# Kernel tuning notes

Hardware: AMD Instinct MI355X
Metric: run time of the kernel (lower is better)

Reference implementation:

```python
import jax, jax.numpy as jnp
import numpy as np
import math

B, S, HID, NH = 2, 1024, 4096, 32
HD = HID // NH  # 128


def setup_inputs() -> dict:
    key = jax.random.key(0)
    ks = jax.random.split(key, 6)
    scale = 0.02
    x = jax.random.normal(ks[0], (B, S, HID), dtype=jnp.float32)
    Wq = jax.random.normal(ks[1], (HID, HID), dtype=jnp.float32) * scale
    Wk = jax.random.normal(ks[2], (HID, HID), dtype=jnp.float32) * scale
    Wv = jax.random.normal(ks[3], (HID, HID), dtype=jnp.float32) * scale
    Wo = jax.random.normal(ks[4], (HID, HID), dtype=jnp.float32) * scale
    bq = jnp.zeros((HID,), jnp.float32)
    bk = jnp.zeros((HID,), jnp.float32)
    bv = jnp.zeros((HID,), jnp.float32)
    bo = jnp.zeros((HID,), jnp.float32)
    position_ids = jnp.tile(jnp.arange(S, dtype=jnp.int32)[None, :], (B, 1))
    # additive causal mask: 0 on/below diagonal, large negative above
    causal = jnp.tril(jnp.ones((S, S), dtype=bool))
    attention_mask = jnp.where(causal, 0.0, -1e9).astype(jnp.float32)[None, None]
    return {"x": x, "Wq": Wq, "bq": bq, "Wk": Wk, "bk": bk, "Wv": Wv,
            "bv": bv, "Wo": Wo, "bo": bo, "position_ids": position_ids,
            "attention_mask": attention_mask}


def _rotate_interleaved(t):
    # stack([-t[..., 1::2], t[..., ::2]], -1).reshape_as(t)
    return jnp.stack([-t[..., 1::2], t[..., ::2]], axis=-1).reshape(t.shape)


def reference(x, Wq, bq, Wk, bk, Wv, bv, Wo, bo, position_ids, attention_mask):
    b, s, _ = x.shape
    q = x @ Wq.T + bq
    k = x @ Wk.T + bk
    v = x @ Wv.T + bv
    # [B, NH, S, HD]
    q = q.reshape(b, s, NH, HD).transpose(0, 2, 1, 3)
    k = k.reshape(b, s, NH, HD).transpose(0, 2, 1, 3)
    v = v.reshape(b, s, NH, HD).transpose(0, 2, 1, 3)
    # RoPE (interleaved pairs), cos/sin recomputed each call as in source
    inv_freq = 1.0 / (10000.0 ** (jnp.arange(0, HD, 2, dtype=jnp.float32) / HD))
    ang = position_ids.astype(jnp.float32)[..., None] * inv_freq  # [B,S,HD/2]
    cos = jnp.repeat(jnp.cos(ang), 2, axis=-1)[:, None]  # [B,1,S,HD]
    sin = jnp.repeat(jnp.sin(ang), 2, axis=-1)[:, None]
    q = q * cos + _rotate_interleaved(q) * sin
    k = k * cos + _rotate_interleaved(k) * sin
    # naive full attention
    scores = jnp.einsum('bhqd,bhkd->bhqk', q, k) / math.sqrt(HD)
    scores = scores + attention_mask
    probs = jax.nn.softmax(scores, axis=-1)
    out = jnp.einsum('bhqk,bhkd->bhqd', probs, v)
    out = out.transpose(0, 2, 1, 3).reshape(b, s, HID)
    return out @ Wo.T + bo
```

## Files before the change

kernel.cpp:

```cpp
#include <hip/hip_runtime.h>
#include <hip/hip_bf16.h>
#include <cmath>

constexpr int cB  = 2;
constexpr int cS  = 1024;
constexpr int cNH = 32;
constexpr int cHD = 128;
constexpr int cHID = 4096;
constexpr int cM  = cB * cS;

typedef unsigned short u16;
typedef __bf16 bf16x8 __attribute__((ext_vector_type(8)));
typedef float  f32x4  __attribute__((ext_vector_type(4)));

__device__ __forceinline__ u16 f2b(float f) { return __builtin_bit_cast(u16, (__bf16)f); }

__global__ void cvt_bf16(const float* __restrict__ in, u16* __restrict__ out, int n8) {
  int i = blockIdx.x * blockDim.x + threadIdx.x;
  if (i >= n8) return;
  const float4* in4 = (const float4*)in;
  float4 a = in4[2 * i], b = in4[2 * i + 1];
  union { u16 u[8]; uint4 v; } r;
  r.u[0] = f2b(a.x); r.u[1] = f2b(a.y); r.u[2] = f2b(a.z); r.u[3] = f2b(a.w);
  r.u[4] = f2b(b.x); r.u[5] = f2b(b.y); r.u[6] = f2b(b.z); r.u[7] = f2b(b.w);
  ((uint4*)out)[i] = r.v;
}

__global__ void rope_table_k(const int* __restrict__ pos,
                             float* __restrict__ cosT, float* __restrict__ sinT) {
  int idx = blockIdx.x * blockDim.x + threadIdx.x;
  int i = idx & 63, bs = idx >> 6;
  float p = (float)pos[bs];
  float freq = exp2f(-(float)i * (13.287712379549449f / 64.0f));
  float a = p * freq;
  float s, c;
  sincosf(a, &s, &c);
  cosT[idx] = c; sinT[idx] = s;
}

__global__ void rope_apply(u16* __restrict__ Q, u16* __restrict__ Kb,
                           const float* __restrict__ cosT, const float* __restrict__ sinT) {
  int idx = blockIdx.x * blockDim.x + threadIdx.x;
  const int nPer = cB * cS * cNH * (cHD / 8);
  u16* P = (idx < nPer) ? Q : Kb;
  int t = (idx < nPer) ? idx : idx - nPer;
  int d8 = t & 15;
  int h  = (t >> 4) & 31;
  int bs = t >> 9;
  size_t base = ((size_t)bs * cNH + h) * cHD + d8 * 8;
  uint4 v = *reinterpret_cast<uint4*>(P + base);
  u16* u = reinterpret_cast<u16*>(&v);
  int pb = bs * 64 + d8 * 4;
  float4 cs = *reinterpret_cast<const float4*>(cosT + pb);
  float4 sn = *reinterpret_cast<const float4*>(sinT + pb);
  float co[4] = {cs.x, cs.y, cs.z, cs.w};
  float si[4] = {sn.x, sn.y, sn.z, sn.w};
#pragma unroll
  for (int p = 0; p < 4; ++p) {
    float e = (float)__builtin_bit_cast(__bf16, u[2 * p]);
    float o = (float)__builtin_bit_cast(__bf16, u[2 * p + 1]);
    float e2 = e * co[p] - o * si[p];
    float o2 = o * co[p] + e * si[p];
    u[2 * p]     = f2b(e2);
    u[2 * p + 1] = f2b(o2);
  }
  *reinterpret_cast<uint4*>(P + base) = v;
}

__global__ void transpose_v(const u16* __restrict__ V, u16* __restrict__ Vt) {
  __shared__ u16 tile[32][33];
  int bh = blockIdx.z;
  int b = bh >> 5, h = bh & 31;
  int s0 = blockIdx.x * 32, d0 = blockIdx.y * 32;
  int tx = threadIdx.x & 31, ty0 = threadIdx.x >> 5;
#pragma unroll
  for (int i = 0; i < 4; ++i) {
    int r = ty0 + i * 8;
    tile[r][tx] = V[((size_t)(b * cS + s0 + r) * cNH + h) * cHD + d0 + tx];
  }
  __syncthreads();
#pragma unroll
  for (int i = 0; i < 4; ++i) {
    int r = ty0 + i * 8;
    Vt[((size_t)bh * cHD + d0 + r) * cS + s0 + tx] = tile[tx][r];
  }
}

template <int MODE>
__global__ __launch_bounds__(256)
void gemm_bt(const u16* __restrict__ A,
             const u16* __restrict__ W0, const u16* __restrict__ W1,
             const u16* __restrict__ W2,
             const float* __restrict__ b0, const float* __restrict__ b1,
             const float* __restrict__ b2,
             void* o0, void* o1, void* o2, int kLen) {
  __shared__ __align__(16) u16 sA[2][128 * 64];
  __shared__ __align__(16) u16 sB[2][128 * 64];
  const int tid = threadIdx.x;
  const int w = tid >> 6, lane = tid & 63;
  const int c = lane & 15, g = lane >> 4;
  const int m0 = blockIdx.x * 128;
  const int gn0 = blockIdx.y * 128;
  const int sel = gn0 >> 12;
  const int n0 = gn0 & 4095;
  const u16* Bw = (sel == 0) ? W0 : (sel == 1 ? W1 : W2);
  const int k0 = blockIdx.z * kLen;
  const int wm = w >> 1, wn = w & 1;

  f32x4 acc[4][4] = {};
  const int nkt = kLen >> 6;

#define STAGE(kt, buf)                                                         \
  {                                                                            \
    _Pragma("unroll") for (int j = 0; j < 4; ++j) {                            \
      int chunk = (j * 4 + w) * 64 + lane;                                     \
      int row = chunk >> 3, lc = chunk & 7;                                    \
      __builtin_amdgcn_global_load_lds(                                        \
          (const void*)(A + (size_t)(m0 + row) * cHID + k0 + (kt) * 64 + lc * 8), \
          (void*)(sA[buf] + (size_t)(j * 4 + w) * 512), 16, 0, 0);             \
      __builtin_amdgcn_global_load_lds(                                        \
          (const void*)(Bw + (size_t)(n0 + row) * cHID + k0 + (kt) * 64 + lc * 8), \
          (void*)(sB[buf] + (size_t)(j * 4 + w) * 512), 16, 0, 0);             \
    }                                                                          \
  }

  STAGE(0, 0);
  __syncthreads();

  for (int kt = 0; kt < nkt; ++kt) {
    const int buf = kt & 1;
    if (kt + 1 < nkt) STAGE(kt + 1, buf ^ 1);

    bf16x8 af[2][4], bfr[2][4];
#pragma unroll
    for (int kf = 0; kf < 2; ++kf) {
#pragma unroll
      for (int f = 0; f < 4; ++f) {
        int ra = wm * 64 + f * 16 + c;
        af[kf][f] = *reinterpret_cast<const bf16x8*>(sA[buf] + ra * 64 + (kf * 4 + g) * 8);
        int rb = wn * 64 + f * 16 + c;
        bfr[kf][f] = *reinterpret_cast<const bf16x8*>(sB[buf] + rb * 64 + (kf * 4 + g) * 8);
      }
    }
#pragma unroll
    for (int kf = 0; kf < 2; ++kf)
#pragma unroll
      for (int mf = 0; mf < 4; ++mf)
#pragma unroll
        for (int nf = 0; nf < 4; ++nf)
          acc[mf][nf] = __builtin_amdgcn_mfma_f32_16x16x32_bf16(af[kf][mf], bfr[kf][nf], acc[mf][nf], 0, 0, 0);

    __syncthreads();
  }
#undef STAGE

  const float* bp = (sel == 0) ? b0 : (sel == 1 ? b1 : b2);
  void* op = (sel == 0) ? o0 : (sel == 1 ? o1 : o2);
  float* fp = (float*)op;
  if (MODE == 2) fp += (size_t)blockIdx.z * cM * cHID;

#pragma unroll
  for (int nf = 0; nf < 4; ++nf) {
    int col = n0 + wn * 64 + nf * 16 + c;
    float bv = (MODE == 2) ? 0.f : bp[col];
#pragma unroll
    for (int mf = 0; mf < 4; ++mf) {
      int row = m0 + wm * 64 + mf * 16 + g * 4;
#pragma unroll
      for (int r = 0; r < 4; ++r) {
        float v = acc[mf][nf][r] + bv;
        if (MODE == 0)
          ((u16*)op)[(size_t)(row + r) * cHID + col] = f2b(v);
        else
          fp[(size_t)(row + r) * cHID + col] = v;
      }
    }
  }
}

__global__ void combine_bias(const float* __restrict__ P,
                             const float* __restrict__ bias,
                             float* __restrict__ out) {
  int i = blockIdx.x * blockDim.x + threadIdx.x;
  float4 a = ((const float4*)P)[i];
  float4 b = ((const float4*)P)[i + (cM * cHID / 4)];
  int col4 = (i & (cHID / 4 - 1)) * 4;
  float4 bb = *reinterpret_cast<const float4*>(bias + col4);
  float4 r;
  r.x = a.x + b.x + bb.x; r.y = a.y + b.y + bb.y;
  r.z = a.z + b.z + bb.z; r.w = a.w + b.w + bb.w;
  ((float4*)out)[i] = r;
}

__global__ __launch_bounds__(256, 2)
void attn_kernel(const u16* __restrict__ Q, const u16* __restrict__ Kb,
                 const u16* __restrict__ Vt, u16* __restrict__ O) {
  __shared__ __align__(16) char sK[2][16384];
  __shared__ __align__(16) char sV[2][16384];
  __shared__ __align__(16) char sP[8192];
  const int tid = threadIdx.x, w = tid >> 6, lane = tid & 63;
  const int c = lane & 15, g = lane >> 4;
  const int bh = blockIdx.y;
  const int b = bh >> 5, h = bh & 31;
  const int NT = cS / 64;
  const int qtA = blockIdx.x, qtB = NT - 1 - blockIdx.x;
  const float kSc = 0.12751744f;

  bf16x8 qf[2][4];
#pragma unroll
  for (int s = 0; s < 2; ++s) {
    int q0s = (s ? qtA : qtB) * 64;
    size_t qrow = ((size_t)(b * cS + q0s + w * 16 + c) * cNH + h) * cHD;
#pragma unroll
    for (int df = 0; df < 4; ++df)
      qf[s][df] = *reinterpret_cast<const bf16x8*>(Q + qrow + df * 32 + g * 8);
  }

  f32x4 o[2][8] = {};
  float mx[2][4], ls[2][4];
#pragma unroll
  for (int s = 0; s < 2; ++s)
#pragma unroll
    for (int r = 0; r < 4; ++r) { mx[s][r] = -1e30f; ls[s][r] = 0.f; }

  uint4 kv[4], vv[4];
#define LOADT(t)                                                               \
  {                                                                            \
    _Pragma("unroll") for (int i = 0; i < 4; ++i) {                            \
      int cidx = i * 256 + tid;                                                \
      { int row = cidx >> 4, ch = cidx & 15;                                   \
        kv[i] = *reinterpret_cast<const uint4*>(                               \
            Kb + ((size_t)(b * cS + (t) * 64 + row) * cNH + h) * cHD + ch * 8); } \
      { int row = cidx >> 3, ch = cidx & 7;                                    \
        vv[i] = *reinterpret_cast<const uint4*>(                               \
            Vt + ((size_t)bh * cHD + row) * cS + (t) * 64 + ch * 8); }         \
    }                                                                          \
  }
#define WRITET(buf)                                                            \
  {                                                                            \
    _Pragma("unroll") for (int i = 0; i < 4; ++i) {                            \
      int cidx = i * 256 + tid;                                                \
      { int row = cidx >> 4, ch = cidx & 15;                                   \
        *reinterpret_cast<uint4*>(sK[buf] + row * 256 + ((ch ^ (row & 7)) * 16)) = kv[i]; } \
      { int row = cidx >> 3, ch = cidx & 7;                                    \
        *reinterpret_cast<uint4*>(sV[buf] + row * 128 + ((ch ^ (row & 7)) * 16)) = vv[i]; } \
    }                                                                          \
  }

  LOADT(0);
  WRITET(0);
  int cur = 0;

  for (int t = 0; t <= qtB; ++t) {
    __syncthreads();
    if (t < qtB) LOADT(t + 1);

#pragma unroll
    for (int s = 0; s < 2; ++s) {
      const int qt_s = s ? qtA : qtB;
      if (t > qt_s) continue;
      const int q0_s = qt_s * 64;

      f32x4 sc[4] = {};
#pragma unroll
      for (int df = 0; df < 4; ++df) {
        bf16x8 kb[4];
#pragma unroll
        for (int cf = 0; cf < 4; ++cf) {
          int kr = cf * 16 + c;
          kb[cf] = *reinterpret_cast<const bf16x8*>(sK[cur] + kr * 256 + (((df * 4 + g) ^ (kr & 7)) * 16));
        }
#pragma unroll
        for (int cf = 0; cf < 4; ++cf)
          sc[cf] = __builtin_amdgcn_mfma_f32_16x16x32_bf16(qf[s][df], kb[cf], sc[cf], 0, 0, 0);
      }

      if (t == qt_s) {
#pragma unroll
        for (int cf = 0; cf < 4; ++cf) {
          int kg = t * 64 + cf * 16 + c;
#pragma unroll
          for (int r = 0; r < 4; ++r) {
            int qg = q0_s + w * 16 + g * 4 + r;
            if (kg > qg) sc[cf][r] = -1e30f;
          }
        }
      }

      float alpha[4];
#pragma unroll
      for (int r = 0; r < 4; ++r) {
        float v = fmaxf(fmaxf(sc[0][r], sc[1][r]), fmaxf(sc[2][r], sc[3][r]));
        v = fmaxf(v, __shfl_xor(v, 1));
        v = fmaxf(v, __shfl_xor(v, 2));
        v = fmaxf(v, __shfl_xor(v, 4));
        v = fmaxf(v, __shfl_xor(v, 8));
        float mn = fmaxf(mx[s][r], v);
        alpha[r] = exp2f((mx[s][r] - mn) * kSc);
        mx[s][r] = mn;
      }
      float rs[4] = {0.f, 0.f, 0.f, 0.f};
#pragma unroll
      for (int cf = 0; cf < 4; ++cf)
#pragma unroll
        for (int r = 0; r < 4; ++r) {
          float p = exp2f((sc[cf][r] - mx[s][r]) * kSc);
          sc[cf][r] = p;
          rs[r] += p;
        }
#pragma unroll
      for (int r = 0; r < 4; ++r) {
        float v = rs[r];
        v += __shfl_xor(v, 1); v += __shfl_xor(v, 2);
        v += __shfl_xor(v, 4); v += __shfl_xor(v, 8);
        ls[s][r] = ls[s][r] * alpha[r] + v;
      }
#pragma unroll
      for (int nf = 0; nf < 8; ++nf)
#pragma unroll
        for (int r = 0; r < 4; ++r)
          o[s][nf][r] *= alpha[r];

      char* myP = sP + w * 2048;
#pragma unroll
      for (int cf = 0; cf < 4; ++cf) {
        int kcol = cf * 16 + c;
        int chunk = kcol >> 3, within = kcol & 7;
#pragma unroll
        for (int r = 0; r < 4; ++r) {
          int qr = g * 4 + r;
          *reinterpret_cast<u16*>(myP + qr * 128 + ((chunk ^ (qr & 7)) * 16) + within * 2) =
              f2b(sc[cf][r]);
        }
      }
      bf16x8 pa[2];
#pragma unroll
      for (int kf = 0; kf < 2; ++kf)
        pa[kf] = *reinterpret_cast<const bf16x8*>(myP + c * 128 + (((kf * 4 + g) ^ (c & 7)) * 16));

#pragma unroll
      for (int kf = 0; kf < 2; ++kf) {
#pragma unroll
        for (int nf = 0; nf < 8; ++nf) {
          int dr = nf * 16 + c;
          bf16x8 vb = *reinterpret_cast<const bf16x8*>(sV[cur] + dr * 128 + (((kf * 4 + g) ^ (dr & 7)) * 16));
          o[s][nf] = __builtin_amdgcn_mfma_f32_16x16x32_bf16(pa[kf], vb, o[s][nf], 0, 0, 0);
        }
      }
    }

    if (t < qtB) { WRITET(cur ^ 1); cur ^= 1; }
  }

  __syncthreads();
#pragma unroll
  for (int s = 0; s < 2; ++s) {
#pragma unroll
    for (int nf = 0; nf < 8; ++nf) {
#pragma unroll
      for (int r = 0; r < 4; ++r) {
        float v = o[s][nf][r] / ls[s][r];
        int qr = w * 16 + g * 4 + r;
        *reinterpret_cast<u16*>(sK[s] + qr * 256 + (nf * 16 + c) * 2) = f2b(v);
      }
    }
  }
  __syncthreads();
#pragma unroll
  for (int s = 0; s < 2; ++s) {
    int q0_s = (s ? qtA : qtB) * 64;
#pragma unroll
    for (int i = 0; i < 4; ++i) {
      int cidx = i * 256 + tid;
      int row = cidx >> 4, ch = cidx & 15;
      uint4 v = *reinterpret_cast<const uint4*>(sK[s] + row * 256 + ch * 16);
      *reinterpret_cast<uint4*>(O + ((size_t)(b * cS + q0_s + row) * cNH + h) * cHD + ch * 8) = v;
    }
  }
#undef LOADT
#undef WRITET
}

extern "C" void kernel_launch(void* const* d_in, const int* in_sizes, int n_in,
                              void* d_out, int out_size, void* d_ws, size_t ws_size,
                              hipStream_t stream) {
  const float* x  = (const float*)d_in[0];
  const float* Wq = (const float*)d_in[1];
  const float* bq = (const float*)d_in[2];
  const float* Wk = (const float*)d_in[3];
  const float* bk = (const float*)d_in[4];
  const float* Wv = (const float*)d_in[5];
  const float* bv = (const float*)d_in[6];
  const float* Wo = (const float*)d_in[7];
  const float* bo = (const float*)d_in[8];
  const int*  pos = (const int*)d_in[9];
  float* out = (float*)d_out;

  char* ws = (char*)d_ws;
  const size_t MB = 1u << 20;
  const int W8 = (cHID * cHID) / 8;
  const int X8 = (cM * cHID) / 8;
  const int R8 = cB * cS * cNH * (cHD / 8);

  if (ws_size >= 168 * MB) {
    u16* xb  = (u16*)(ws);
    u16* Qb  = (u16*)(ws + 16 * MB);
    u16* Kb  = (u16*)(ws + 32 * MB);
    u16* Vb  = (u16*)(ws + 48 * MB);
    float* cosT = (float*)(ws + 64 * MB);
    float* sinT = cosT + cB * cS * 64;
    u16* WbQ = (u16*)(ws + 72 * MB);
    u16* WbK = (u16*)(ws + 104 * MB);
    u16* WbV = (u16*)(ws + 136 * MB);
    u16* Vt  = WbQ;
    u16* Ab  = WbK;
    u16* WbO = WbV;
    float* P01 = (float*)(ws);

    cvt_bf16<<<X8 / 256, 256, 0, stream>>>(x, xb, X8);
    cvt_bf16<<<W8 / 256, 256, 0, stream>>>(Wq, WbQ, W8);
    cvt_bf16<<<W8 / 256, 256, 0, stream>>>(Wk, WbK, W8);
    cvt_bf16<<<W8 / 256, 256, 0, stream>>>(Wv, WbV, W8);
    rope_table_k<<<(cB * cS * 64) / 256, 256, 0, stream>>>(pos, cosT, sinT);

    gemm_bt<0><<<dim3(16, 96), 256, 0, stream>>>(
        xb, WbQ, WbK, WbV, bq, bk, bv, Qb, Kb, Vb, cHID);

    rope_apply<<<(2 * R8) / 256, 256, 0, stream>>>(Qb, Kb, cosT, sinT);
    transpose_v<<<dim3(cS / 32, cHD / 32, cB * cNH), 256, 0, stream>>>(Vb, Vt);
    attn_kernel<<<dim3(cS / 128, cB * cNH), 256, 0, stream>>>(Qb, Kb, Vt, Ab);

    cvt_bf16<<<W8 / 256, 256, 0, stream>>>(Wo, WbO, W8);
    gemm_bt<2><<<dim3(16, 32, 2), 256, 0, stream>>>(
        Ab, WbO, WbO, WbO, nullptr, nullptr, nullptr, P01, P01, P01, cHID / 2);
    combine_bias<<<(cM * cHID / 4) / 256, 256, 0, stream>>>(P01, bo, out);
  } else {
    u16* xb = (u16*)(ws);
    u16* Wb = (u16*)(ws + 16 * MB);
    u16* Qb = (u16*)(ws + 48 * MB);
    u16* Kb = (u16*)(ws + 64 * MB);
    u16* Vb = (u16*)(ws + 80 * MB);
    u16* Vt = xb;
    u16* Ab = Vb;
    float* cosT = (float*)(ws + 96 * MB);
    float* sinT = cosT + cB * cS * 64;

    cvt_bf16<<<X8 / 256, 256, 0, stream>>>(x, xb, X8);
    cvt_bf16<<<W8 / 256, 256, 0, stream>>>(Wq, Wb, W8);
    gemm_bt<0><<<dim3(16, 32), 256, 0, stream>>>(
        xb, Wb, Wb, Wb, bq, bq, bq, Qb, Qb, Qb, cHID);
    cvt_bf16<<<W8 / 256, 256, 0, stream>>>(Wk, Wb, W8);
    gemm_bt<0><<<dim3(16, 32), 256, 0, stream>>>(
        xb, Wb, Wb, Wb, bk, bk, bk, Kb, Kb, Kb, cHID);
    cvt_bf16<<<W8 / 256, 256, 0, stream>>>(Wv, Wb, W8);
    gemm_bt<0><<<dim3(16, 32), 256, 0, stream>>>(
        xb, Wb, Wb, Wb, bv, bv, bv, Vb, Vb, Vb, cHID);

    rope_table_k<<<(cB * cS * 64) / 256, 256, 0, stream>>>(pos, cosT, sinT);
    rope_apply<<<(2 * R8) / 256, 256, 0, stream>>>(Qb, Kb, cosT, sinT);
    transpose_v<<<dim3(cS / 32, cHD / 32, cB * cNH), 256, 0, stream>>>(Vb, Vt);
    attn_kernel<<<dim3(cS / 128, cB * cNH), 256, 0, stream>>>(Qb, Kb, Vt, Ab);

    cvt_bf16<<<W8 / 256, 256, 0, stream>>>(Wo, Wb, W8);
    gemm_bt<1><<<dim3(16, 32), 256, 0, stream>>>(
        Ab, Wb, Wb, Wb, bo, bo, bo, out, out, out, cHID);
  }
}
```

Measured before the change: 550.4 us.

## Rewrite GEMM as 8-wave 128x256 tile with swizzled LDS and split-phase pipeline

Replaces the 256-thread 128x128 GEMM with a 512-thread, 8-wave kernel on 128x256 tiles. LDS chunks are XOR-swizzled to avoid bank conflicts. The main loop waits with explicit vmcnt/lgkmcnt, raw barriers and setprio, and splits the MFMA work into two halves so the second B-fragment reads overlap the first MFMAs. The output projection drops split-K and the combine_bias pass and writes the fp32 result with bias directly, which cuts an extra kernel and its memory traffic but leaves fewer blocks (256) for that GEMM.

```diff
diff --git a/kernel.cpp b/kernel.cpp
--- a/kernel.cpp
+++ b/kernel.cpp
@@ -87,82 +87,117 @@
 }
 
 template <int MODE>
-__global__ __launch_bounds__(256)
-void gemm_bt(const u16* __restrict__ A,
-             const u16* __restrict__ W0, const u16* __restrict__ W1,
-             const u16* __restrict__ W2,
-             const float* __restrict__ b0, const float* __restrict__ b1,
-             const float* __restrict__ b2,
-             void* o0, void* o1, void* o2, int kLen) {
+__global__ __launch_bounds__(512, 2)
+void gemm8(const u16* __restrict__ A,
+           const u16* __restrict__ W0, const u16* __restrict__ W1,
+           const u16* __restrict__ W2,
+           const float* __restrict__ b0, const float* __restrict__ b1,
+           const float* __restrict__ b2,
+           void* o0, void* o1, void* o2) {
   __shared__ __align__(16) u16 sA[2][128 * 64];
-  __shared__ __align__(16) u16 sB[2][128 * 64];
+  __shared__ __align__(16) u16 sB[2][256 * 64];
   const int tid = threadIdx.x;
-  const int w = tid >> 6, lane = tid & 63;
+  const int wid = tid >> 6, lane = tid & 63;
   const int c = lane & 15, g = lane >> 4;
+  const int wm = wid >> 2, wn = wid & 3;
   const int m0 = blockIdx.x * 128;
-  const int gn0 = blockIdx.y * 128;
+  const int gn0 = blockIdx.y * 256;
   const int sel = gn0 >> 12;
   const int n0 = gn0 & 4095;
   const u16* Bw = (sel == 0) ? W0 : (sel == 1 ? W1 : W2);
-  const int k0 = blockIdx.z * kLen;
-  const int wm = w >> 1, wn = w & 1;
 
   f32x4 acc[4][4] = {};
-  const int nkt = kLen >> 6;
-
-#define STAGE(kt, buf)                                                         \
+  const int nkt = cHID / 64;
+
+#define STAGE8(kt, bf)                                                         \
   {                                                                            \
-    _Pragma("unroll") for (int j = 0; j < 4; ++j) {                            \
-      int chunk = (j * 4 + w) * 64 + lane;                                     \
-      int row = chunk >> 3, lc = chunk & 7;                                    \
+    _Pragma("unroll") for (int l = 0; l < 2; ++l) {                            \
+      int chunk = (l * 8 + wid) * 64 + lane;                                   \
+      int row = chunk >> 3, kc = (chunk & 7) ^ (row & 7);                      \
       __builtin_amdgcn_global_load_lds(                                        \
-          (const void*)(A + (size_t)(m0 + row) * cHID + k0 + (kt) * 64 + lc * 8), \
-          (void*)(sA[buf] + (size_t)(j * 4 + w) * 512), 16, 0, 0);             \
+          (const void*)(A + (size_t)(m0 + row) * cHID + (kt) * 64 + kc * 8),   \
+          (void*)(&sA[bf][(l * 8 + wid) * 512]), 16, 0, 0);                    \
+    }                                                                          \
+    _Pragma("unroll") for (int l = 0; l < 4; ++l) {                            \
+      int chunk = (l * 8 + wid) * 64 + lane;                                   \
+      int row = chunk >> 3, kc = (chunk & 7) ^ (row & 7);                      \
       __builtin_amdgcn_global_load_lds(                                        \
-          (const void*)(Bw + (size_t)(n0 + row) * cHID + k0 + (kt) * 64 + lc * 8), \
-          (void*)(sB[buf] + (size_t)(j * 4 + w) * 512), 16, 0, 0);             \
+          (const void*)(Bw + (size_t)(n0 + row) * cHID + (kt) * 64 + kc * 8),  \
+          (void*)(&sB[bf][(l * 8 + wid) * 512]), 16, 0, 0);                    \
     }                                                                          \
   }
 
-  STAGE(0, 0);
-  __syncthreads();
-
+  STAGE8(0, 0);
   for (int kt = 0; kt < nkt; ++kt) {
     const int buf = kt & 1;
-    if (kt + 1 < nkt) STAGE(kt + 1, buf ^ 1);
-
-    bf16x8 af[2][4], bfr[2][4];
-#pragma unroll
-    for (int kf = 0; kf < 2; ++kf) {
-#pragma unroll
-      for (int f = 0; f < 4; ++f) {
-        int ra = wm * 64 + f * 16 + c;
-        af[kf][f] = *reinterpret_cast<const bf16x8*>(sA[buf] + ra * 64 + (kf * 4 + g) * 8);
-        int rb = wn * 64 + f * 16 + c;
-        bfr[kf][f] = *reinterpret_cast<const bf16x8*>(sB[buf] + rb * 64 + (kf * 4 + g) * 8);
-      }
+    if (kt + 1 < nkt) {
+      STAGE8(kt + 1, buf ^ 1);
+      asm volatile("s_waitcnt vmcnt(6)" ::: "memory");
+    } else {
+      asm volatile("s_waitcnt vmcnt(0)" ::: "memory");
     }
-#pragma unroll
-    for (int kf = 0; kf < 2; ++kf)
+    __builtin_amdgcn_sched_barrier(0);
+    __builtin_amdgcn_s_barrier();
+
+    bf16x8 a[4][2], b[2][2];
+#pragma unroll
+    for (int mf = 0; mf < 4; ++mf)
+#pragma unroll
+      for (int kk = 0; kk < 2; ++kk) {
+        int ra = wm * 64 + mf * 16 + c;
+        a[mf][kk] = *reinterpret_cast<const bf16x8*>(
+            &sA[buf][ra * 64 + (((kk * 4 + g) ^ (ra & 7)) * 8)]);
+      }
+#pragma unroll
+    for (int nf = 0; nf < 2; ++nf)
+#pragma unroll
+      for (int kk = 0; kk < 2; ++kk) {
+        int rb = wn * 64 + nf * 16 + c;
+        b[nf][kk] = *reinterpret_cast<const bf16x8*>(
+            &sB[buf][rb * 64 + (((kk * 4 + g) ^ (rb & 7)) * 8)]);
+      }
+    __builtin_amdgcn_s_barrier();
+    asm volatile("s_waitcnt lgkmcnt(0)" ::: "memory");
+    __builtin_amdgcn_sched_barrier(0);
+    __builtin_amdgcn_s_setprio(1);
+#pragma unroll
+    for (int kk = 0; kk < 2; ++kk)
 #pragma unroll
       for (int mf = 0; mf < 4; ++mf)
 #pragma unroll
-        for (int nf = 0; nf < 4; ++nf)
-          acc[mf][nf] = __builtin_amdgcn_mfma_f32_16x16x32_bf16(af[kf][mf], bfr[kf][nf], acc[mf][nf], 0, 0, 0);
-
-    __syncthreads();
-  }
-#undef STAGE
+        for (int nf = 0; nf < 2; ++nf)
+          acc[mf][nf] = __builtin_amdgcn_mfma_f32_16x16x32_bf16(a[mf][kk], b[nf][kk], acc[mf][nf], 0, 0, 0);
+    __builtin_amdgcn_s_setprio(0);
+
+#pragma unroll
+    for (int nf = 0; nf < 2; ++nf)
+#pragma unroll
+      for (int kk = 0; kk < 2; ++kk) {
+        int rb = wn * 64 + (nf + 2) * 16 + c;
+        b[nf][kk] = *reinterpret_cast<const bf16x8*>(
+            &sB[buf][rb * 64 + (((kk * 4 + g) ^ (rb & 7)) * 8)]);
+      }
+    asm volatile("s_waitcnt lgkmcnt(0)" ::: "memory");
+    __builtin_amdgcn_sched_barrier(0);
+    __builtin_amdgcn_s_barrier();
+    __builtin_amdgcn_s_setprio(1);
+#pragma unroll
+    for (int kk = 0; kk < 2; ++kk)
+#pragma unroll
+      for (int mf = 0; mf < 4; ++mf)
+#pragma unroll
+        for (int nf = 0; nf < 2; ++nf)
+          acc[mf][nf + 2] = __builtin_amdgcn_mfma_f32_16x16x32_bf16(a[mf][kk], b[nf][kk], acc[mf][nf + 2], 0, 0, 0);
+    __builtin_amdgcn_s_setprio(0);
+  }
+#undef STAGE8
 
   const float* bp = (sel == 0) ? b0 : (sel == 1 ? b1 : b2);
   void* op = (sel == 0) ? o0 : (sel == 1 ? o1 : o2);
-  float* fp = (float*)op;
-  if (MODE == 2) fp += (size_t)blockIdx.z * cM * cHID;
-
 #pragma unroll
   for (int nf = 0; nf < 4; ++nf) {
     int col = n0 + wn * 64 + nf * 16 + c;
-    float bv = (MODE == 2) ? 0.f : bp[col];
+    float bv = bp[col];
 #pragma unroll
     for (int mf = 0; mf < 4; ++mf) {
       int row = m0 + wm * 64 + mf * 16 + g * 4;
@@ -172,24 +207,10 @@
         if (MODE == 0)
           ((u16*)op)[(size_t)(row + r) * cHID + col] = f2b(v);
         else
-          fp[(size_t)(row + r) * cHID + col] = v;
+          ((float*)op)[(size_t)(row + r) * cHID + col] = v;
       }
     }
   }
-}
-
-__global__ void combine_bias(const float* __restrict__ P,
-                             const float* __restrict__ bias,
-                             float* __restrict__ out) {
-  int i = blockIdx.x * blockDim.x + threadIdx.x;
-  float4 a = ((const float4*)P)[i];
-  float4 b = ((const float4*)P)[i + (cM * cHID / 4)];
-  int col4 = (i & (cHID / 4 - 1)) * 4;
-  float4 bb = *reinterpret_cast<const float4*>(bias + col4);
-  float4 r;
-  r.x = a.x + b.x + bb.x; r.y = a.y + b.y + bb.y;
-  r.z = a.z + b.z + bb.z; r.w = a.w + b.w + bb.w;
-  ((float4*)out)[i] = r;
 }
 
 __global__ __launch_bounds__(256, 2)
@@ -415,7 +436,6 @@
     u16* Vt  = WbQ;
     u16* Ab  = WbK;
     u16* WbO = WbV;
-    float* P01 = (float*)(ws);
 
     cvt_bf16<<<X8 / 256, 256, 0, stream>>>(x, xb, X8);
     cvt_bf16<<<W8 / 256, 256, 0, stream>>>(Wq, WbQ, W8);
@@ -423,17 +443,16 @@
     cvt_bf16<<<W8 / 256, 256, 0, stream>>>(Wv, WbV, W8);
     rope_table_k<<<(cB * cS * 64) / 256, 256, 0, stream>>>(pos, cosT, sinT);
 
-    gemm_bt<0><<<dim3(16, 96), 256, 0, stream>>>(
-        xb, WbQ, WbK, WbV, bq, bk, bv, Qb, Kb, Vb, cHID);
+    gemm8<0><<<dim3(16, 48), 512, 0, stream>>>(
+        xb, WbQ, WbK, WbV, bq, bk, bv, Qb, Kb, Vb);
 
     rope_apply<<<(2 * R8) / 256, 256, 0, stream>>>(Qb, Kb, cosT, sinT);
     transpose_v<<<dim3(cS / 32, cHD / 32, cB * cNH), 256, 0, stream>>>(Vb, Vt);
     attn_kernel<<<dim3(cS / 128, cB * cNH), 256, 0, stream>>>(Qb, Kb, Vt, Ab);
 
     cvt_bf16<<<W8 / 256, 256, 0, stream>>>(Wo, WbO, W8);
-    gemm_bt<2><<<dim3(16, 32, 2), 256, 0, stream>>>(
-        Ab, WbO, WbO, WbO, nullptr, nullptr, nullptr, P01, P01, P01, cHID / 2);
-    combine_bias<<<(cM * cHID / 4) / 256, 256, 0, stream>>>(P01, bo, out);
+    gemm8<1><<<dim3(16, 16), 512, 0, stream>>>(
+        Ab, WbO, WbO, WbO, bo, bo, bo, out, out, out);
   } else {
     u16* xb = (u16*)(ws);
     u16* Wb = (u16*)(ws + 16 * MB);
@@ -447,14 +466,14 @@
 
     cvt_bf16<<<X8 / 256, 256, 0, stream>>>(x, xb, X8);
     cvt_bf16<<<W8 / 256, 256, 0, stream>>>(Wq, Wb, W8);
-    gemm_bt<0><<<dim3(16, 32), 256, 0, stream>>>(
-        xb, Wb, Wb, Wb, bq, bq, bq, Qb, Qb, Qb, cHID);
+    gemm8<0><<<dim3(16, 16), 512, 0, stream>>>(
+        xb, Wb, Wb, Wb, bq, bq, bq, Qb, Qb, Qb);
     cvt_bf16<<<W8 / 256, 256, 0, stream>>>(Wk, Wb, W8);
-    gemm_bt<0><<<dim3(16, 32), 256, 0, stream>>>(
-        xb, Wb, Wb, Wb, bk, bk, bk, Kb, Kb, Kb, cHID);
+    gemm8<0><<<dim3(16, 16), 512, 0, stream>>>(
+        xb, Wb, Wb, Wb, bk, bk, bk, Kb, Kb, Kb);
     cvt_bf16<<<W8 / 256, 256, 0, stream>>>(Wv, Wb, W8);
-    gemm_bt<0><<<dim3(16, 32), 256, 0, stream>>>(
-        xb, Wb, Wb, Wb, bv, bv, bv, Vb, Vb, Vb, cHID);
+    gemm8<0><<<dim3(16, 16), 512, 0, stream>>>(
+        xb, Wb, Wb, Wb, bv, bv, bv, Vb, Vb, Vb);
 
     rope_table_k<<<(cB * cS * 64) / 256, 256, 0, stream>>>(pos, cosT, sinT);
     rope_apply<<<(2 * R8) / 256, 256, 0, stream>>>(Qb, Kb, cosT, sinT);
@@ -462,7 +481,7 @@
     attn_kernel<<<dim3(cS / 128, cB * cNH), 256, 0, stream>>>(Qb, Kb, Vt, Ab);
 
     cvt_bf16<<<W8 / 256, 256, 0, stream>>>(Wo, Wb, W8);
-    gemm_bt<1><<<dim3(16, 32), 256, 0, stream>>>(
-        Ab, Wb, Wb, Wb, bo, bo, bo, out, out, out, cHID);
-  }
-}
+    gemm8<1><<<dim3(16, 16), 512, 0, stream>>>(
+        Ab, Wb, Wb, Wb, bo, bo, bo, out, out, out);
+  }
+}
```

Result: slower. 567.0 us (+3.0%).
